# Kernel tuning notes

Measured on AMD Instinct MI355X. Metric: run time of the kernel, lower is better.

## Reference

```python
import jax, jax.numpy as jnp
import numpy as np

D_S = 1024
N_HEADS = 16
HEAD_DIM = D_S // N_HEADS
FFN_DIM = 4096
B, S = 2, 1024
LN_EPS = 1e-5


def _layernorm(x, gamma, beta):
    mu = jnp.mean(x, axis=-1, keepdims=True)
    var = jnp.var(x, axis=-1, keepdims=True)
    return (x - mu) * jax.lax.rsqrt(var + LN_EPS) * gamma + beta


def _mish(x):
    return x * jnp.tanh(jax.nn.softplus(x))


def setup_inputs() -> dict:
    key = jax.random.key(0)
    ks = jax.random.split(key, 12)
    std = 1.0 / np.sqrt(D_S)
    return {
        "x": jax.random.normal(ks[0], (B, S, D_S), jnp.float32),
        "attn_bias": jax.random.normal(ks[1], (B, N_HEADS, S, S), jnp.float32),
        "ln1_g": jnp.ones((D_S,), jnp.float32),
        "ln1_b": jnp.zeros((D_S,), jnp.float32),
        "Wqkv": jax.random.normal(ks[2], (D_S, 3 * D_S), jnp.float32) * std,
        "bqkv": jax.random.normal(ks[3], (3 * D_S,), jnp.float32) * 0.02,
        "Wo": jax.random.normal(ks[4], (D_S, D_S), jnp.float32) * std,
        "bo": jax.random.normal(ks[5], (D_S,), jnp.float32) * 0.02,
        "ln2_g": jnp.ones((D_S,), jnp.float32),
        "ln2_b": jnp.zeros((D_S,), jnp.float32),
        "W1": jax.random.normal(ks[6], (D_S, FFN_DIM), jnp.float32) * std,
        "b1": jax.random.normal(ks[7], (FFN_DIM,), jnp.float32) * 0.02,
        "W2": jax.random.normal(ks[8], (FFN_DIM, D_S), jnp.float32) * (1.0 / np.sqrt(FFN_DIM)),
        "b2": jax.random.normal(ks[9], (D_S,), jnp.float32) * 0.02,
    }


def reference(x, attn_bias, ln1_g, ln1_b, Wqkv, bqkv, Wo, bo, ln2_g, ln2_b, W1, b1, W2, b2):
    b, s, d = x.shape
    h = _layernorm(x, ln1_g, ln1_b)
    qkv = (h @ Wqkv + bqkv).reshape(b, s, 3, N_HEADS, HEAD_DIM)
    q, k, v = qkv[:, :, 0], qkv[:, :, 1], qkv[:, :, 2]  # [B,S,H,hd]
    scale = HEAD_DIM ** -0.5
    # scores: [B,H,S,S]
    scores = jnp.einsum("bqhd,bkhd->bhqk", q, k) * scale + attn_bias
    attn = jax.nn.softmax(scores, axis=-1)
    ctx = jnp.einsum("bhqk,bkhd->bqhd", attn, v).reshape(b, s, d)
    x = x + (ctx @ Wo + bo)
    h2 = _layernorm(x, ln2_g, ln2_b)
    ffn = _mish(h2 @ W1 + b1) @ W2 + b2
    return x + ffn
```

## Files before the change

### kernel.cpp

```cpp
#include <hip/hip_runtime.h>


typedef __attribute__((ext_vector_type(8))) __bf16 bf16x8;
typedef __attribute__((ext_vector_type(4))) float  f32x4;

__device__ __forceinline__ unsigned short f2bf(float f) {
  unsigned int u = __builtin_bit_cast(unsigned int, f);
  u += 0x7fffu + ((u >> 16) & 1u);
  return (unsigned short)(u >> 16);
}

__device__ __forceinline__ void gload16(const void* g, void* l) {
  __builtin_amdgcn_global_load_lds(
      (const __attribute__((address_space(1))) void*)g,
      (__attribute__((address_space(3))) void*)l, 16, 0, 0);
}

__global__ void convert_transpose(const float* __restrict__ W,
                                  unsigned short* __restrict__ Wt,
                                  int K, int N) {
  __shared__ float tile[32][33];
  const int n0 = blockIdx.x * 32, k0 = blockIdx.y * 32;
  const int tx = threadIdx.x, ty = threadIdx.y;
#pragma unroll
  for (int r = 0; r < 4; ++r)
    tile[ty + 8 * r][tx] = W[(size_t)(k0 + ty + 8 * r) * N + n0 + tx];
  __syncthreads();
#pragma unroll
  for (int r = 0; r < 4; ++r)
    Wt[(size_t)(n0 + ty + 8 * r) * K + k0 + tx] = f2bf(tile[tx][ty + 8 * r]);
}

__global__ __launch_bounds__(256) void ln_kernel(const float* __restrict__ in,
                                                 const float* __restrict__ g,
                                                 const float* __restrict__ b,
                                                 unsigned short* __restrict__ out) {
  const int row = blockIdx.x;
  const int t = threadIdx.x;
  const float4 v = reinterpret_cast<const float4*>(in + (size_t)row * 1024)[t];
  float s  = v.x + v.y + v.z + v.w;
  float s2 = v.x * v.x + v.y * v.y + v.z * v.z + v.w * v.w;
#pragma unroll
  for (int m = 1; m < 64; m <<= 1) { s += __shfl_xor(s, m); s2 += __shfl_xor(s2, m); }
  __shared__ float ps[4], ps2[4];
  const int wv = t >> 6;
  if ((t & 63) == 0) { ps[wv] = s; ps2[wv] = s2; }
  __syncthreads();
  float ts = 0.f, ts2 = 0.f;
#pragma unroll
  for (int i = 0; i < 4; ++i) { ts += ps[i]; ts2 += ps2[i]; }
  const float mu = ts * (1.f / 1024.f);
  const float var = ts2 * (1.f / 1024.f) - mu * mu;
  const float rstd = rsqrtf(var + 1e-5f);
  const float4 gg = reinterpret_cast<const float4*>(g)[t];
  const float4 bb = reinterpret_cast<const float4*>(b)[t];
  ushort4 ov;
  ov.x = f2bf((v.x - mu) * rstd * gg.x + bb.x);
  ov.y = f2bf((v.y - mu) * rstd * gg.y + bb.y);
  ov.z = f2bf((v.z - mu) * rstd * gg.z + bb.z);
  ov.w = f2bf((v.w - mu) * rstd * gg.w + bb.w);
  *reinterpret_cast<ushort4*>(out + (size_t)row * 1024 + t * 4) = ov;
}

template <int MODE, int BN>
__global__ __launch_bounds__(256, 2) void gemm_kernel(
    const unsigned short* __restrict__ A, const unsigned short* __restrict__ Bt,
    const float* __restrict__ bias, int M, int N, int K,
    float* __restrict__ outf, const float* __restrict__ res,
    unsigned short* __restrict__ outb,
    unsigned short* __restrict__ kbuf, unsigned short* __restrict__ vtbuf) {
  constexpr int BM = 128, BK = 64;
  constexpr int WN = (BN == 128) ? 2 : 1;
  constexpr int WM = 4 / WN;
  constexpr int WR = BM / WM / 16;
  constexpr int WC = BN / WN / 16;
  __shared__ unsigned short a_sh[BM * BK];
  __shared__ unsigned short b_sh[BN * BK];

  const int tid = threadIdx.x;
  const int wave = tid >> 6, lane = tid & 63;
  const int wm = wave / WN, wn = wave % WN;
  const int l15 = lane & 15, l4 = lane >> 4;

  const int nwg = gridDim.x, cpx = nwg >> 3;
  const int swz = (blockIdx.x & 7) * cpx + (blockIdx.x >> 3);
  const int GY = M / BM;
  const long bm0 = (long)(swz % GY) * BM;
  const long bn0 = (long)(swz / GY) * BN;

  const int sr8 = lane >> 3;
  const int gc  = ((lane & 7) ^ sr8) * 8;

  const unsigned short* agp[BM / 32];
  const unsigned short* bgp[BN / 32];
  unsigned short* alb[BM / 32];
  unsigned short* blb[BN / 32];
#pragma unroll
  for (int i = 0; i < BM / 32; ++i) {
    const int r = wave * (BM / 4) + i * 8;
    agp[i] = A + (bm0 + r + sr8) * (long)K + gc;
    alb[i] = &a_sh[r * BK];
  }
#pragma unroll
  for (int i = 0; i < BN / 32; ++i) {
    const int r = wave * (BN / 4) + i * 8;
    bgp[i] = Bt + (bn0 + r + sr8) * (long)K + gc;
    blb[i] = &b_sh[r * BK];
  }

  f32x4 acc[WR][WC] = {};

  for (int k0 = 0; k0 < K; k0 += BK) {
    __syncthreads();
#pragma unroll
    for (int i = 0; i < BM / 32; ++i) gload16(agp[i] + k0, alb[i]);
#pragma unroll
    for (int i = 0; i < BN / 32; ++i) gload16(bgp[i] + k0, blb[i]);
    asm volatile("s_waitcnt vmcnt(0)" ::: "memory");
    __syncthreads();

#pragma unroll
    for (int kk = 0; kk < 2; ++kk) {
      bf16x8 af[WR], bfr[WC];
#pragma unroll
      for (int mf = 0; mf < WR; ++mf) {
        const int r = wm * (BM / WM) + mf * 16 + l15;
        const int c = ((kk * 4 + l4) ^ (r & 7)) * 8;
        af[mf] = *reinterpret_cast<const bf16x8*>(&a_sh[r * BK + c]);
      }
#pragma unroll
      for (int nf = 0; nf < WC; ++nf) {
        const int r = wn * (BN / WN) + nf * 16 + l15;
        const int c = ((kk * 4 + l4) ^ (r & 7)) * 8;
        bfr[nf] = *reinterpret_cast<const bf16x8*>(&b_sh[r * BK + c]);
      }
#pragma unroll
      for (int mf = 0; mf < WR; ++mf)
#pragma unroll
        for (int nf = 0; nf < WC; ++nf)
          acc[mf][nf] = __builtin_amdgcn_mfma_f32_16x16x32_bf16(af[mf], bfr[nf], acc[mf][nf], 0, 0, 0);
    }
  }

#pragma unroll
  for (int mf = 0; mf < WR; ++mf) {
#pragma unroll
    for (int nf = 0; nf < WC; ++nf) {
#pragma unroll
      for (int r = 0; r < 4; ++r) {
        const long row = bm0 + wm * (BM / WM) + mf * 16 + 4 * l4 + r;
        const long col = bn0 + wn * (BN / WN) + nf * 16 + l15;
        float v = acc[mf][nf][r] + bias[col];
        if constexpr (MODE == 0) {
          const int n = (int)col;
          const int which = n >> 10, rem = n & 1023;
          const int head = rem >> 6, d = rem & 63;
          const int b = (int)(row >> 10), s = (int)(row & 1023);
          const unsigned short bv = f2bf(v);
          const long qi = ((long)(b * 16 + head) * 1024 + s) * 64 + d;
          if (which == 0)      outb[qi] = bv;
          else if (which == 1) kbuf[qi] = bv;
          else                 vtbuf[((long)(b * 16 + head) * 64 + d) * 1024 + s] = bv;
        } else if constexpr (MODE == 1) {
          outf[row * N + col] = v + res[row * N + col];
        } else if constexpr (MODE == 2) {
          float mv;
          if (v > 20.f) mv = v;
          else { const float t = __expf(v); const float u = t * t + 2.f * t;
                 mv = v * u / (u + 2.f); }
          outb[row * (long)N + col] = f2bf(mv);
        } else {
          outf[row * N + col] = v + res[row * N + col];
        }
      }
    }
  }
}

__global__ __launch_bounds__(256, 3) void attn_kernel(
    const unsigned short* __restrict__ qb, const unsigned short* __restrict__ kb,
    const unsigned short* __restrict__ vtb, const float* __restrict__ bias,
    unsigned short* __restrict__ ctx) {
  constexpr int S = 1024;
  __shared__ unsigned short k_sh[2][64 * 64];
  __shared__ unsigned short vt_sh[2][64 * 64];
  __shared__ unsigned short p_sh[4][16 * 72];

  const int bh = blockIdx.y;
  const int q0 = blockIdx.x * 64;
  const int tid = threadIdx.x, wave = tid >> 6, lane = tid & 63;
  const int l15 = lane & 15, l4 = lane >> 4;

  const long qbase = ((long)bh * S + q0 + wave * 16 + l15) * 64;
  const bf16x8 qf0 = *reinterpret_cast<const bf16x8*>(qb + qbase + 8 * l4);
  const bf16x8 qf1 = *reinterpret_cast<const bf16x8*>(qb + qbase + 8 * l4 + 32);

  const int sr8 = lane >> 3;
  const int gchunk = ((lane & 7) ^ sr8) * 8;

  const long kbase = (long)bh * S * 64;
  const long vbase = (long)bh * 64 * S;

  const float* bB = bias + ((long)bh * S + q0 + wave * 16 + 4 * l4) * S + l15;

  f32x4 oacc[4] = {};
  float lacc[4] = {};
  float ba[4][4], bb2[4][4];

  auto stageKV = [&](int kv, int buf) {
#pragma unroll
    for (int i = 0; i < 2; ++i) {
      const int r = i * 32 + wave * 8;
      gload16(kb + kbase + (long)(kv + r + sr8) * 64 + gchunk, &k_sh[buf][r * 64]);
      gload16(vtb + vbase + (long)(r + sr8) * S + kv + gchunk, &vt_sh[buf][r * 64]);
    }
  };

  stageKV(0, 0);
#pragma unroll
  for (int r = 0; r < 4; ++r)
#pragma unroll
    for (int nf = 0; nf < 4; ++nf)
      ba[r][nf] = bB[(long)r * S + nf * 16];
  asm volatile("s_waitcnt vmcnt(0)" ::: "memory");
  __syncthreads();

#pragma unroll 1
  for (int tt = 0; tt < 8; ++tt) {
    const int t0 = 2 * tt;
#pragma unroll
    for (int half = 0; half < 2; ++half) {
      const int t = t0 + half;
      const int cur = half, nxt = half ^ 1;
      float (*bcur)[4] = half ? bb2 : ba;
      float (*bnxt)[4] = half ? ba : bb2;

      if (t < 15) stageKV((t + 1) * 64, nxt);

      f32x4 sc[4];
#pragma unroll
      for (int nf = 0; nf < 4; ++nf) {
        const int r = nf * 16 + l15;
        const bf16x8 kf0 = *reinterpret_cast<const bf16x8*>(
            &k_sh[cur][r * 64 + ((l4) ^ (r & 7)) * 8]);
        const bf16x8 kf1 = *reinterpret_cast<const bf16x8*>(
            &k_sh[cur][r * 64 + ((l4 + 4) ^ (r & 7)) * 8]);
        f32x4 z = {};
        z = __builtin_amdgcn_mfma_f32_16x16x32_bf16(qf0, kf0, z, 0, 0, 0);
        sc[nf] = __builtin_amdgcn_mfma_f32_16x16x32_bf16(qf1, kf1, z, 0, 0, 0);
      }

      if (t < 15) {
        const float* bn = bB + (t + 1) * 64;
#pragma unroll
        for (int r = 0; r < 4; ++r)
#pragma unroll
          for (int nf = 0; nf < 4; ++nf)
            bnxt[r][nf] = bn[(long)r * S + nf * 16];
      }

      float pv[4][4];
#pragma unroll
      for (int r = 0; r < 4; ++r) {
        float ls = 0.f;
#pragma unroll
        for (int nf = 0; nf < 4; ++nf) {
          const float p = __expf(sc[nf][r] * 0.125f + bcur[r][nf]);
          pv[nf][r] = p;
          ls += p;
        }
        lacc[r] += ls;
      }

#pragma unroll
      for (int nf = 0; nf < 4; ++nf)
#pragma unroll
        for (int r = 0; r < 4; ++r)
          p_sh[wave][(4 * l4 + r) * 72 + nf * 16 + l15] = f2bf(pv[nf][r]);

      const bf16x8 pa0 = *reinterpret_cast<const bf16x8*>(&p_sh[wave][l15 * 72 + 8 * l4]);
      const bf16x8 pa1 = *reinterpret_cast<const bf16x8*>(&p_sh[wave][l15 * 72 + 8 * l4 + 32]);
#pragma unroll
      for (int nf = 0; nf < 4; ++nf) {
        const int r = nf * 16 + l15;
        const bf16x8 vf0 = *reinterpret_cast<const bf16x8*>(
            &vt_sh[cur][r * 64 + ((l4) ^ (r & 7)) * 8]);
        const bf16x8 vf1 = *reinterpret_cast<const bf16x8*>(
            &vt_sh[cur][r * 64 + ((l4 + 4) ^ (r & 7)) * 8]);
        oacc[nf] = __builtin_amdgcn_mfma_f32_16x16x32_bf16(pa0, vf0, oacc[nf], 0, 0, 0);
        oacc[nf] = __builtin_amdgcn_mfma_f32_16x16x32_bf16(pa1, vf1, oacc[nf], 0, 0, 0);
      }

      asm volatile("s_waitcnt vmcnt(0)" ::: "memory");
      __syncthreads();
    }
  }

#pragma unroll
  for (int r = 0; r < 4; ++r) {
    float v = lacc[r];
    v += __shfl_xor(v, 1);
    v += __shfl_xor(v, 2);
    v += __shfl_xor(v, 4);
    v += __shfl_xor(v, 8);
    lacc[r] = 1.f / v;
  }

  const int b = bh >> 4, h = bh & 15;
#pragma unroll
  for (int nf = 0; nf < 4; ++nf)
#pragma unroll
    for (int r = 0; r < 4; ++r) {
      const long s = q0 + wave * 16 + 4 * l4 + r;
      const long col = h * 64 + nf * 16 + l15;
      ctx[((long)b * S + s) * 1024 + col] = f2bf(oacc[nf][r] * lacc[r]);
    }
}

extern "C" void kernel_launch(void* const* d_in, const int* in_sizes, int n_in,
                              void* d_out, int out_size, void* d_ws, size_t ws_size,
                              hipStream_t stream) {
  const float* x    = (const float*)d_in[0];
  const float* ab   = (const float*)d_in[1];
  const float* ln1g = (const float*)d_in[2];
  const float* ln1b = (const float*)d_in[3];
  const float* Wqkv = (const float*)d_in[4];
  const float* bqkv = (const float*)d_in[5];
  const float* Wo   = (const float*)d_in[6];
  const float* bo   = (const float*)d_in[7];
  const float* ln2g = (const float*)d_in[8];
  const float* ln2b = (const float*)d_in[9];
  const float* W1   = (const float*)d_in[10];
  const float* b1   = (const float*)d_in[11];
  const float* W2   = (const float*)d_in[12];
  const float* b2   = (const float*)d_in[13];
  float* out = (float*)d_out;

  char* ws = (char*)d_ws;
  size_t off = 0;
  auto alloc = [&](size_t bytes) {
    char* p = ws + off;
    off += (bytes + 255) & ~(size_t)255;
    return p;
  };
  unsigned short* wqkv_t = (unsigned short*)alloc((size_t)3072 * 1024 * 2);
  unsigned short* wo_t   = (unsigned short*)alloc((size_t)1024 * 1024 * 2);
  unsigned short* w1_t   = (unsigned short*)alloc((size_t)4096 * 1024 * 2);
  unsigned short* w2_t   = (unsigned short*)alloc((size_t)4096 * 1024 * 2);
  unsigned short* h1     = (unsigned short*)alloc((size_t)2048 * 1024 * 2);
  unsigned short* qbuf   = (unsigned short*)alloc((size_t)2048 * 1024 * 2);
  unsigned short* kbuf   = (unsigned short*)alloc((size_t)2048 * 1024 * 2);
  unsigned short* vtbuf  = (unsigned short*)alloc((size_t)2048 * 1024 * 2);
  unsigned short* ctx    = (unsigned short*)alloc((size_t)2048 * 1024 * 2);
  unsigned short* h2     = (unsigned short*)alloc((size_t)2048 * 1024 * 2);
  float*          r1     = (float*)alloc((size_t)2048 * 1024 * 4);
  unsigned short* ffn1   = h1;
  (void)ws_size; (void)in_sizes; (void)n_in; (void)out_size;

  const dim3 tb(32, 8);
  convert_transpose<<<dim3(3072 / 32, 1024 / 32), tb, 0, stream>>>(Wqkv, wqkv_t, 1024, 3072);
  convert_transpose<<<dim3(1024 / 32, 1024 / 32), tb, 0, stream>>>(Wo, wo_t, 1024, 1024);
  convert_transpose<<<dim3(4096 / 32, 1024 / 32), tb, 0, stream>>>(W1, w1_t, 1024, 4096);
  convert_transpose<<<dim3(1024 / 32, 4096 / 32), tb, 0, stream>>>(W2, w2_t, 4096, 1024);

  ln_kernel<<<2048, 256, 0, stream>>>(x, ln1g, ln1b, h1);

  gemm_kernel<0, 128><<<384, 256, 0, stream>>>(h1, wqkv_t, bqkv, 2048, 3072, 1024,
                                               nullptr, nullptr, qbuf, kbuf, vtbuf);

  attn_kernel<<<dim3(16, 32), 256, 0, stream>>>(qbuf, kbuf, vtbuf, ab, ctx);

  gemm_kernel<1, 64><<<256, 256, 0, stream>>>(ctx, wo_t, bo, 2048, 1024, 1024,
                                              r1, x, nullptr, nullptr, nullptr);

  ln_kernel<<<2048, 256, 0, stream>>>(r1, ln2g, ln2b, h2);

  gemm_kernel<2, 128><<<512, 256, 0, stream>>>(h2, w1_t, b1, 2048, 4096, 1024,
                                               nullptr, nullptr, ffn1, nullptr, nullptr);

  gemm_kernel<3, 64><<<256, 256, 0, stream>>>(ffn1, w2_t, b2, 2048, 1024, 4096,
                                              out, r1, nullptr, nullptr, nullptr);
}
```

Before: 196.2 us.

## Double-buffer GEMM tiles, merge weight conversions, enlarge attention blocks, retile N=1024 GEMMs

The GEMM main loop now double-buffers its LDS tiles, so the next K-slice is loaded while MFMAs run on the current one, with one barrier per iteration. The four weight convert-transpose launches become a single kernel, cutting launch overhead. Attention now uses 512-thread blocks covering 128 queries, which shares each K/V tile across more waves. The Wo and W2 GEMMs switch to 64x64 tiles to launch more workgroups. The trade-offs are twice the GEMM LDS footprint and possibly lower occupancy for the larger attention blocks.

Measured after the change: 178.4 us. -9.1%, faster.

```diff
diff --git a/kernel.cpp b/kernel.cpp
--- a/kernel.cpp
+++ b/kernel.cpp
@@ -16,11 +16,20 @@
       (__attribute__((address_space(3))) void*)l, 16, 0, 0);
 }
 
-__global__ void convert_transpose(const float* __restrict__ W,
-                                  unsigned short* __restrict__ Wt,
-                                  int K, int N) {
+__global__ void convert_all(const float* __restrict__ Wqkv, const float* __restrict__ Wo,
+                            const float* __restrict__ W1, const float* __restrict__ W2,
+                            unsigned short* __restrict__ wqkv_t, unsigned short* __restrict__ wo_t,
+                            unsigned short* __restrict__ w1_t, unsigned short* __restrict__ w2_t) {
+  const int id = blockIdx.x;
+  const float* W; unsigned short* Wt; int K, N, t;
+  if (id < 3072)      { W = Wqkv; Wt = wqkv_t; K = 1024; N = 3072; t = id; }
+  else if (id < 4096) { W = Wo;   Wt = wo_t;   K = 1024; N = 1024; t = id - 3072; }
+  else if (id < 8192) { W = W1;   Wt = w1_t;   K = 1024; N = 4096; t = id - 4096; }
+  else                { W = W2;   Wt = w2_t;   K = 4096; N = 1024; t = id - 8192; }
+  const int nx = N >> 5;
+  const int n0 = (t % nx) * 32, k0 = (t / nx) * 32;
+
   __shared__ float tile[32][33];
-  const int n0 = blockIdx.x * 32, k0 = blockIdx.y * 32;
   const int tx = threadIdx.x, ty = threadIdx.y;
 #pragma unroll
   for (int r = 0; r < 4; ++r)
@@ -62,20 +71,21 @@
   *reinterpret_cast<ushort4*>(out + (size_t)row * 1024 + t * 4) = ov;
 }
 
-template <int MODE, int BN>
+template <int MODE, int BM, int BN>
 __global__ __launch_bounds__(256, 2) void gemm_kernel(
     const unsigned short* __restrict__ A, const unsigned short* __restrict__ Bt,
     const float* __restrict__ bias, int M, int N, int K,
     float* __restrict__ outf, const float* __restrict__ res,
     unsigned short* __restrict__ outb,
     unsigned short* __restrict__ kbuf, unsigned short* __restrict__ vtbuf) {
-  constexpr int BM = 128, BK = 64;
-  constexpr int WN = (BN == 128) ? 2 : 1;
+  constexpr int BK = 64;
+  constexpr int WN = (BN >= 128 || BM == 64) ? 2 : 1;
   constexpr int WM = 4 / WN;
   constexpr int WR = BM / WM / 16;
   constexpr int WC = BN / WN / 16;
-  __shared__ unsigned short a_sh[BM * BK];
-  __shared__ unsigned short b_sh[BN * BK];
+  constexpr int AI = BM / 32, BI = BN / 32;
+  __shared__ unsigned short a_sh[2][BM * BK];
+  __shared__ unsigned short b_sh[2][BN * BK];
 
   const int tid = threadIdx.x;
   const int wave = tid >> 6, lane = tid & 63;
@@ -91,33 +101,39 @@
   const int sr8 = lane >> 3;
   const int gc  = ((lane & 7) ^ sr8) * 8;
 
-  const unsigned short* agp[BM / 32];
-  const unsigned short* bgp[BN / 32];
-  unsigned short* alb[BM / 32];
-  unsigned short* blb[BN / 32];
-#pragma unroll
-  for (int i = 0; i < BM / 32; ++i) {
+  const unsigned short* agp[AI];
+  const unsigned short* bgp[BI];
+  int aoff[AI], boff[BI];
+#pragma unroll
+  for (int i = 0; i < AI; ++i) {
     const int r = wave * (BM / 4) + i * 8;
     agp[i] = A + (bm0 + r + sr8) * (long)K + gc;
-    alb[i] = &a_sh[r * BK];
-  }
-#pragma unroll
-  for (int i = 0; i < BN / 32; ++i) {
+    aoff[i] = r * BK;
+  }
+#pragma unroll
+  for (int i = 0; i < BI; ++i) {
     const int r = wave * (BN / 4) + i * 8;
     bgp[i] = Bt + (bn0 + r + sr8) * (long)K + gc;
-    blb[i] = &b_sh[r * BK];
-  }
+    boff[i] = r * BK;
+  }
+
+  auto stage = [&](int buf, int k0) {
+#pragma unroll
+    for (int i = 0; i < AI; ++i) gload16(agp[i] + k0, &a_sh[buf][aoff[i]]);
+#pragma unroll
+    for (int i = 0; i < BI; ++i) gload16(bgp[i] + k0, &b_sh[buf][boff[i]]);
+  };
 
   f32x4 acc[WR][WC] = {};
 
-  for (int k0 = 0; k0 < K; k0 += BK) {
-    __syncthreads();
-#pragma unroll
-    for (int i = 0; i < BM / 32; ++i) gload16(agp[i] + k0, alb[i]);
-#pragma unroll
-    for (int i = 0; i < BN / 32; ++i) gload16(bgp[i] + k0, blb[i]);
-    asm volatile("s_waitcnt vmcnt(0)" ::: "memory");
-    __syncthreads();
+  stage(0, 0);
+  asm volatile("s_waitcnt vmcnt(0)" ::: "memory");
+  __syncthreads();
+
+  const int NT = K / BK;
+  for (int t = 0; t < NT; ++t) {
+    const int cur = t & 1;
+    if (t + 1 < NT) stage(cur ^ 1, (t + 1) * BK);
 
 #pragma unroll
     for (int kk = 0; kk < 2; ++kk) {
@@ -126,13 +142,13 @@
       for (int mf = 0; mf < WR; ++mf) {
         const int r = wm * (BM / WM) + mf * 16 + l15;
         const int c = ((kk * 4 + l4) ^ (r & 7)) * 8;
-        af[mf] = *reinterpret_cast<const bf16x8*>(&a_sh[r * BK + c]);
+        af[mf] = *reinterpret_cast<const bf16x8*>(&a_sh[cur][r * BK + c]);
       }
 #pragma unroll
       for (int nf = 0; nf < WC; ++nf) {
         const int r = wn * (BN / WN) + nf * 16 + l15;
         const int c = ((kk * 4 + l4) ^ (r & 7)) * 8;
-        bfr[nf] = *reinterpret_cast<const bf16x8*>(&b_sh[r * BK + c]);
+        bfr[nf] = *reinterpret_cast<const bf16x8*>(&b_sh[cur][r * BK + c]);
       }
 #pragma unroll
       for (int mf = 0; mf < WR; ++mf)
@@ -140,6 +156,9 @@
         for (int nf = 0; nf < WC; ++nf)
           acc[mf][nf] = __builtin_amdgcn_mfma_f32_16x16x32_bf16(af[mf], bfr[nf], acc[mf][nf], 0, 0, 0);
     }
+
+    asm volatile("s_waitcnt vmcnt(0)" ::: "memory");
+    __syncthreads();
   }
 
 #pragma unroll
@@ -166,7 +185,7 @@
         } else if constexpr (MODE == 2) {
           float mv;
           if (v > 20.f) mv = v;
-          else { const float t = __expf(v); const float u = t * t + 2.f * t;
+          else { const float t2 = __expf(v); const float u = t2 * t2 + 2.f * t2;
                  mv = v * u / (u + 2.f); }
           outb[row * (long)N + col] = f2bf(mv);
         } else {
@@ -177,17 +196,17 @@
   }
 }
 
-__global__ __launch_bounds__(256, 3) void attn_kernel(
+__global__ __launch_bounds__(512, 2) void attn_kernel(
     const unsigned short* __restrict__ qb, const unsigned short* __restrict__ kb,
     const unsigned short* __restrict__ vtb, const float* __restrict__ bias,
     unsigned short* __restrict__ ctx) {
   constexpr int S = 1024;
   __shared__ unsigned short k_sh[2][64 * 64];
   __shared__ unsigned short vt_sh[2][64 * 64];
-  __shared__ unsigned short p_sh[4][16 * 72];
+  __shared__ unsigned short p_sh[8][16 * 72];
 
   const int bh = blockIdx.y;
-  const int q0 = blockIdx.x * 64;
+  const int q0 = blockIdx.x * 128;
   const int tid = threadIdx.x, wave = tid >> 6, lane = tid & 63;
   const int l15 = lane & 15, l4 = lane >> 4;
 
@@ -197,7 +216,6 @@
 
   const int sr8 = lane >> 3;
   const int gchunk = ((lane & 7) ^ sr8) * 8;
-
   const long kbase = (long)bh * S * 64;
   const long vbase = (long)bh * 64 * S;
 
@@ -208,12 +226,9 @@
   float ba[4][4], bb2[4][4];
 
   auto stageKV = [&](int kv, int buf) {
-#pragma unroll
-    for (int i = 0; i < 2; ++i) {
-      const int r = i * 32 + wave * 8;
-      gload16(kb + kbase + (long)(kv + r + sr8) * 64 + gchunk, &k_sh[buf][r * 64]);
-      gload16(vtb + vbase + (long)(r + sr8) * S + kv + gchunk, &vt_sh[buf][r * 64]);
-    }
+    const int r = wave * 8;
+    gload16(kb + kbase + (long)(kv + r + sr8) * 64 + gchunk, &k_sh[buf][r * 64]);
+    gload16(vtb + vbase + (long)(r + sr8) * S + kv + gchunk, &vt_sh[buf][r * 64]);
   };
 
   stageKV(0, 0);
@@ -357,27 +372,24 @@
   unsigned short* ffn1   = h1;
   (void)ws_size; (void)in_sizes; (void)n_in; (void)out_size;
 
-  const dim3 tb(32, 8);
-  convert_transpose<<<dim3(3072 / 32, 1024 / 32), tb, 0, stream>>>(Wqkv, wqkv_t, 1024, 3072);
-  convert_transpose<<<dim3(1024 / 32, 1024 / 32), tb, 0, stream>>>(Wo, wo_t, 1024, 1024);
-  convert_transpose<<<dim3(4096 / 32, 1024 / 32), tb, 0, stream>>>(W1, w1_t, 1024, 4096);
-  convert_transpose<<<dim3(1024 / 32, 4096 / 32), tb, 0, stream>>>(W2, w2_t, 4096, 1024);
+  convert_all<<<12288, dim3(32, 8), 0, stream>>>(Wqkv, Wo, W1, W2,
+                                                 wqkv_t, wo_t, w1_t, w2_t);
 
   ln_kernel<<<2048, 256, 0, stream>>>(x, ln1g, ln1b, h1);
 
-  gemm_kernel<0, 128><<<384, 256, 0, stream>>>(h1, wqkv_t, bqkv, 2048, 3072, 1024,
-                                               nullptr, nullptr, qbuf, kbuf, vtbuf);
-
-  attn_kernel<<<dim3(16, 32), 256, 0, stream>>>(qbuf, kbuf, vtbuf, ab, ctx);
-
-  gemm_kernel<1, 64><<<256, 256, 0, stream>>>(ctx, wo_t, bo, 2048, 1024, 1024,
-                                              r1, x, nullptr, nullptr, nullptr);
+  gemm_kernel<0, 128, 128><<<384, 256, 0, stream>>>(h1, wqkv_t, bqkv, 2048, 3072, 1024,
+                                                    nullptr, nullptr, qbuf, kbuf, vtbuf);
+
+  attn_kernel<<<dim3(8, 32), 512, 0, stream>>>(qbuf, kbuf, vtbuf, ab, ctx);
+
+  gemm_kernel<1, 64, 64><<<512, 256, 0, stream>>>(ctx, wo_t, bo, 2048, 1024, 1024,
+                                                  r1, x, nullptr, nullptr, nullptr);
 
   ln_kernel<<<2048, 256, 0, stream>>>(r1, ln2g, ln2b, h2);
 
-  gemm_kernel<2, 128><<<512, 256, 0, stream>>>(h2, w1_t, b1, 2048, 4096, 1024,
-                                               nullptr, nullptr, ffn1, nullptr, nullptr);
-
-  gemm_kernel<3, 64><<<256, 256, 0, stream>>>(ffn1, w2_t, b2, 2048, 1024, 4096,
-                                              out, r1, nullptr, nullptr, nullptr);
-}
+  gemm_kernel<2, 128, 128><<<512, 256, 0, stream>>>(h2, w1_t, b1, 2048, 4096, 1024,
+                                                    nullptr, nullptr, ffn1, nullptr, nullptr);
+
+  gemm_kernel<3, 64, 64><<<512, 256, 0, stream>>>(ffn1, w2_t, b2, 2048, 1024, 4096,
+                                                  out, r1, nullptr, nullptr, nullptr);
+}
```
